# Performance work log

Hardware: AMD Instinct MI355X
Metric: run time of the kernel (lower is better)

The kernel has to match this reference:

```python
import jax, jax.numpy as jnp
import numpy as np

N = 100000        # nodes
E = 1600000       # edges
D = 128           # feature dim (all layers)
G = 128           # graphs
C = 10            # num_classes
L = 3             # conv layers
EPS = 1e-5
SLOPE = 0.03


def setup_inputs() -> dict:
    key = jax.random.key(0)
    ks = jax.random.split(key, 12)
    x = jax.random.normal(ks[0], (N, D), dtype=jnp.float32)
    edge_index = jax.random.randint(ks[1], (2, E), 0, N, dtype=jnp.int64)
    batch = jnp.sort(jax.random.randint(ks[2], (N,), 0, G, dtype=jnp.int64))
    s = 1.0 / np.sqrt(D)
    Wc = jax.random.uniform(ks[3], (L, D, D), jnp.float32, -s, s)
    bc = jax.random.uniform(ks[4], (L, D), jnp.float32, -s, s)
    bn_gamma = jnp.ones((2, D), jnp.float32)
    bn_beta = jnp.zeros((2, D), jnp.float32)
    bn_mean = jax.random.normal(ks[5], (2, D), jnp.float32) * 0.1
    bn_var = jax.random.uniform(ks[6], (2, D), jnp.float32, 0.5, 1.5)
    lin_w = jax.random.uniform(ks[7], (C, D), jnp.float32, -s, s)
    lin_b = jax.random.uniform(ks[8], (C,), jnp.float32, -s, s)
    return {"x": x, "edge_index": edge_index, "batch": batch, "Wc": Wc,
            "bc": bc, "bn_gamma": bn_gamma, "bn_beta": bn_beta,
            "bn_mean": bn_mean, "bn_var": bn_var, "lin_w": lin_w, "lin_b": lin_b}


def _gcn_norm(edge_index):
    # add self-loops, compute D^{-1/2}[row] * D^{-1/2}[col] (PyG gcn_norm)
    loops = jnp.arange(N, dtype=edge_index.dtype)
    row = jnp.concatenate([edge_index[0], loops])
    col = jnp.concatenate([edge_index[1], loops])
    deg = jax.ops.segment_sum(jnp.ones_like(col, dtype=jnp.float32), col, num_segments=N)
    dis = jnp.where(deg > 0, jax.lax.rsqrt(deg), 0.0)
    return row, col, dis[row] * dis[col]


def reference(x, edge_index, batch, Wc, bc, bn_gamma, bn_beta, bn_mean, bn_var, lin_w, lin_b):
    row, col, norm = _gcn_norm(edge_index)
    h = x
    for i in range(L):
        h = h @ Wc[i]                                          # linear transform [N, D]
        msg = h[row] * norm[:, None]                           # gather + normalize [E+N, D]
        h = jax.ops.segment_sum(msg, col, num_segments=N) + bc[i]
        if i < 2:  # batchnorm only for i < len(batchnorms)-1 (eval mode, running stats)
            h = (h - bn_mean[i]) * jax.lax.rsqrt(bn_var[i] + EPS) * bn_gamma[i] + bn_beta[i]
        h = jnp.where(h > 0, h, SLOPE * h)                     # LeakyReLU(0.03)
    # global mean pool over graphs
    counts = jax.ops.segment_sum(jnp.ones((N,), jnp.float32), batch, num_segments=G)
    pooled = jax.ops.segment_sum(h, batch, num_segments=G) / jnp.maximum(counts, 1.0)[:, None]
    # dropout is identity in eval; final linear head
    return pooled @ lin_w.T + lin_b                            # [G, C]
```

## Files before the change

### kernel.cpp

```cpp
#include <hip/hip_runtime.h>
#include <hip/hip_bf16.h>

#define NN 100000
#define EE 1600000
#define DD 128
#define GG 128
#define CC 10
#define NPB 256
#define NB 391
#define SCAP 5120
#define VPT 16
#define CPAD 32
#define PPN 64

typedef __attribute__((ext_vector_type(8))) short bf16x8;
typedef __attribute__((ext_vector_type(4))) float f32x4;
typedef __attribute__((ext_vector_type(2))) float f32x2;
typedef unsigned int u32;

__device__ inline float blo(u32 u) { return __uint_as_float(u << 16); }
__device__ inline float bhi(u32 u) { return __uint_as_float(u & 0xffff0000u); }
__device__ inline u32 bpack(float x, float y) {
    u32 bx = __float_as_uint(x);
    u32 by = __float_as_uint(y);
    bx = (bx + 0x7fffu + ((bx >> 16) & 1u)) >> 16;
    by = (by + 0x7fffu + ((by >> 16) & 1u)) & 0xffff0000u;
    return bx | by;
}

__global__ __launch_bounds__(256) void k_bcount(const int* __restrict__ col,
                                                int* __restrict__ bhist) {
    __shared__ int lh[NB];
    int tid = threadIdx.x;
    for (int b = tid; b < NB; b += 256) lh[b] = 0;
    __syncthreads();
    int base = blockIdx.x * (256 * VPT);
#pragma unroll
    for (int j = 0; j < VPT; j++) {
        int e = base + j * 256 + tid;
        if (e < EE) atomicAdd(&lh[col[e] >> 8], 1);
    }
    __syncthreads();
    for (int b = tid; b < NB; b += 256) {
        int h = lh[b];
        if (h) atomicAdd(&bhist[b * CPAD], h);
    }
}

__global__ __launch_bounds__(512) void k_bscan(const int* __restrict__ bhist,
                                               int* __restrict__ boffs,
                                               int* __restrict__ bcur) {
    __shared__ int s[512];
    int tid = threadIdx.x;
    int c = (tid < NB) ? bhist[tid * CPAD] : 0;
    s[tid] = c;
    __syncthreads();
    for (int off = 1; off < 512; off <<= 1) {
        int v = (tid >= off) ? s[tid - off] : 0;
        __syncthreads();
        s[tid] += v;
        __syncthreads();
    }
    int excl = s[tid] - c;
    if (tid < NB) {
        boffs[tid] = excl;
        bcur[tid * CPAD] = excl;
    }
    if (tid == NB - 1) boffs[NB] = excl + c;
}

__global__ __launch_bounds__(256) void k_part(const int* __restrict__ row, const int* __restrict__ col,
                                              int* __restrict__ bcur, u32* __restrict__ pairs) {
    __shared__ int lhist[NB];
    __shared__ int gbase[NB];
    __shared__ int lcur[NB];
    int tid = threadIdx.x;
    for (int b = tid; b < NB; b += 256) lhist[b] = 0;
    __syncthreads();
    int base = blockIdx.x * (256 * VPT);
    u32 v[VPT];
    int bb[VPT];
#pragma unroll
    for (int j = 0; j < VPT; j++) {
        int e = base + j * 256 + tid;
        if (e < EE) {
            int r = row[e], c = col[e];
            v[j] = ((u32)r << 8) | (u32)(c & 255);
            bb[j] = c >> 8;
            atomicAdd(&lhist[bb[j]], 1);
        } else {
            bb[j] = -1;
        }
    }
    __syncthreads();
    for (int b = tid; b < NB; b += 256) {
        int h = lhist[b];
        gbase[b] = h ? atomicAdd(&bcur[b * CPAD], h) : 0;
        lcur[b] = 0;
    }
    __syncthreads();
#pragma unroll
    for (int j = 0; j < VPT; j++) {
        if (bb[j] >= 0) {
            int slot = gbase[bb[j]] + atomicAdd(&lcur[bb[j]], 1);
            pairs[slot] = v[j];
        }
    }
}

__global__ __launch_bounds__(256) void k_sort(const u32* __restrict__ pairs,
                                              const int* __restrict__ boffs,
                                              int* __restrict__ offs,
                                              float* __restrict__ dis,
                                              int* __restrict__ src) {
    int b = blockIdx.x;
    int tid = threadIdx.x;
    int nstart = b << 8;
    int nvalid = NN - nstart;
    if (nvalid > NPB) nvalid = NPB;
    int base = boffs[b];
    int eend = boffs[b + 1];
    int cnt = eend - base;
    __shared__ int lcnt[NPB];
    __shared__ int lscan[NPB];
    __shared__ int lcur[NPB];
    __shared__ int lsrc[SCAP];
    lcnt[tid] = 0;
    __syncthreads();
    for (int e = base + tid; e < eend; e += 256)
        atomicAdd(&lcnt[pairs[e] & 255u], 1);
    __syncthreads();
    int c = lcnt[tid];
    lscan[tid] = c;
    __syncthreads();
    for (int off = 1; off < 256; off <<= 1) {
        int v = (tid >= off) ? lscan[tid - off] : 0;
        __syncthreads();
        lscan[tid] += v;
        __syncthreads();
    }
    int excl = lscan[tid] - c;
    if (tid < nvalid) {
        offs[nstart + tid] = base + excl;
        dis[nstart + tid] = rsqrtf((float)(c + 1));
    }
    if (b == NB - 1 && tid == 255) offs[NN] = EE;
    lcur[tid] = excl;
    __syncthreads();
    if (cnt <= SCAP) {
        for (int e = base + tid; e < eend; e += 256) {
            u32 v = pairs[e];
            int slot = atomicAdd(&lcur[v & 255u], 1);
            lsrc[slot] = (int)(v >> 8);
        }
        __syncthreads();
        for (int i = tid; i < cnt; i += 256)
            src[base + i] = lsrc[i];
    } else {
        for (int e = base + tid; e < eend; e += 256) {
            u32 v = pairs[e];
            int slot = base + atomicAdd(&lcur[v & 255u], 1);
            src[slot] = (int)(v >> 8);
        }
    }
}

__global__ void k_prep(const float* __restrict__ Wc, const float* __restrict__ bc,
                       const float* __restrict__ gamma, const float* __restrict__ beta,
                       const float* __restrict__ mean, const float* __restrict__ var,
                       __hip_bfloat16* __restrict__ WT,
                       float* __restrict__ tc) {
    int i = blockIdx.x * 256 + threadIdx.x;
    if (i < 3 * 128) {
        int l = i >> 7, d = i & 127;
        float t;
        if (l < 2) {
            float s = gamma[l * 128 + d] * rsqrtf(var[l * 128 + d] + 1e-5f);
            t = (bc[l * 128 + d] - mean[l * 128 + d]) * s + beta[l * 128 + d];
        } else {
            t = bc[2 * 128 + d];
        }
        tc[i] = t;
    }
    if (i < 3 * 16384) {
        int l = i >> 14, r = (i >> 7) & 127, k = i & 127;
        float s = 1.f;
        if (l < 2) s = gamma[l * 128 + r] * rsqrtf(var[l * 128 + r] + 1e-5f);
        WT[i] = __float2bfloat16(Wc[l * 16384 + k * 128 + r] * s);
    }
}

__global__ __launch_bounds__(256) void k_pre(const float* __restrict__ x,
                                             const float* __restrict__ dis,
                                             u32* __restrict__ hs) {
    int i = blockIdx.x * 256 + threadIdx.x;
    if (i < NN * 64) {
        float dn = dis[i >> 6];
        float2 v = ((const float2*)x)[i];
        hs[i] = bpack(v.x * dn, v.y * dn);
    }
}

template <int PRESCALE>
__global__ __launch_bounds__(1024) void k_aggT(const u32* __restrict__ hin,
                                               const int* __restrict__ offs,
                                               const int* __restrict__ src,
                                               const float* __restrict__ dis,
                                               const __hip_bfloat16* __restrict__ WT,
                                               const float* __restrict__ tc,
                                               u32* __restrict__ hout) {
    __shared__ u32   Atile[16][68];
    __shared__ float Otile[16][132];
    int wid = threadIdx.x >> 6;
    int lane = threadIdx.x & 63;
    int node = blockIdx.x * 16 + wid;
    int e0 = __builtin_amdgcn_readfirstlane(offs[node]);
    int e1 = __builtin_amdgcn_readfirstlane(offs[node + 1]);
    u32 self = hin[((u32)node << 6) + lane];
    f32x2 acc = {blo(self), bhi(self)};
    int e = e0;
    for (; e + 16 <= e1; e += 16) {
        u32 u[16];
#pragma unroll
        for (int j = 0; j < 16; j++) {
            u32 s = (u32)src[e + j];
            u[j] = hin[(s << 6) + lane];
        }
#pragma unroll
        for (int j = 0; j < 16; j++) {
            f32x2 v = {blo(u[j]), bhi(u[j])};
            acc += v;
        }
    }
    for (; e + 8 <= e1; e += 8) {
        u32 u[8];
#pragma unroll
        for (int j = 0; j < 8; j++) {
            u32 s = (u32)src[e + j];
            u[j] = hin[(s << 6) + lane];
        }
#pragma unroll
        for (int j = 0; j < 8; j++) {
            f32x2 v = {blo(u[j]), bhi(u[j])};
            acc += v;
        }
    }
    for (; e < e1; e++) {
        u32 u = hin[((u32)src[e] << 6) + lane];
        f32x2 v = {blo(u), bhi(u)};
        acc += v;
    }
    float dn = dis[node];
    Atile[wid][lane] = bpack(acc.x * dn, acc.y * dn);
    __syncthreads();
    if (wid < 8) {
        int lg = lane >> 4, lr = lane & 15;
        f32x4 c4 = {0.f, 0.f, 0.f, 0.f};
#pragma unroll
        for (int kk = 0; kk < 4; kk++) {
            bf16x8 a = *(const bf16x8*)&Atile[lr][kk * 16 + lg * 4];
            bf16x8 b = *(const bf16x8*)(WT + (size_t)(wid * 16 + lr) * 128 + kk * 32 + lg * 8);
            c4 = __builtin_amdgcn_mfma_f32_16x16x32_bf16(a, b, c4, 0, 0, 0);
        }
#pragma unroll
        for (int r = 0; r < 4; r++)
            Otile[lg * 4 + r][wid * 16 + lr] = c4[r];
    }
    __syncthreads();
    int d0 = lane * 2;
    float r0 = Otile[wid][d0]     + tc[d0];
    float r1 = Otile[wid][d0 + 1] + tc[d0 + 1];
    r0 = r0 > 0.f ? r0 : 0.03f * r0;
    r1 = r1 > 0.f ? r1 : 0.03f * r1;
    if (PRESCALE) { r0 *= dn; r1 *= dn; }
    hout[((u32)node << 6) + lane] = bpack(r0, r1);
}

__global__ __launch_bounds__(64) void k_pool(const u32* __restrict__ h,
                                             const int* __restrict__ batch,
                                             float* __restrict__ pooled,
                                             float* __restrict__ counts) {
    int lane = threadIdx.x;
    int n0 = blockIdx.x * PPN;
    if (n0 >= NN) return;
    int n1 = n0 + PPN;
    if (n1 > NN) n1 = NN;
    float a0 = 0.f, a1 = 0.f, cnt = 0.f;
    int g = batch[n0];
    for (int n = n0; n < n1; n++) {
        int bg = batch[n];
        if (bg != g) {
            atomicAdd(&pooled[g * 128 + lane * 2], a0);
            atomicAdd(&pooled[g * 128 + lane * 2 + 1], a1);
            if (lane == 0) atomicAdd(&counts[g], cnt);
            a0 = 0.f; a1 = 0.f; cnt = 0.f; g = bg;
        }
        u32 u = h[(u32)n * 64u + lane];
        a0 += blo(u); a1 += bhi(u);
        cnt += 1.f;
    }
    atomicAdd(&pooled[g * 128 + lane * 2], a0);
    atomicAdd(&pooled[g * 128 + lane * 2 + 1], a1);
    if (lane == 0) atomicAdd(&counts[g], cnt);
}

__global__ void k_head(const float* __restrict__ pooled, const float* __restrict__ counts,
                       const float* __restrict__ w, const float* __restrict__ b,
                       float* __restrict__ out) {
    int i = blockIdx.x * blockDim.x + threadIdx.x;
    if (i >= GG * CC) return;
    int g = i / CC, c = i % CC;
    float cnt = counts[g];
    cnt = cnt > 1.f ? cnt : 1.f;
    float inv = 1.f / cnt;
    const float* p = &pooled[g * 128];
    const float* ww = &w[c * 128];
    float acc = 0.f;
    for (int d = 0; d < 128; d++) acc += p[d] * ww[d];
    out[i] = acc * inv + b[c];
}

extern "C" void kernel_launch(void* const* d_in, const int* in_sizes, int n_in,
                              void* d_out, int out_size, void* d_ws, size_t ws_size,
                              hipStream_t stream) {
    const float* x     = (const float*)d_in[0];
    const int*   ei    = (const int*)d_in[1];
    const int*   row   = ei;
    const int*   col   = ei + EE;
    const int*   batch = (const int*)d_in[2];
    const float* Wc    = (const float*)d_in[3];
    const float* bc    = (const float*)d_in[4];
    const float* gamma = (const float*)d_in[5];
    const float* beta  = (const float*)d_in[6];
    const float* mean  = (const float*)d_in[7];
    const float* var   = (const float*)d_in[8];
    const float* lw    = (const float*)d_in[9];
    const float* lb    = (const float*)d_in[10];
    float* out = (float*)d_out;

    char* p = (char*)d_ws;
    auto alloc = [&](size_t bytes) -> char* {
        char* r = p;
        p += (bytes + 255) & ~(size_t)255;
        return r;
    };
    float* dis    = (float*)alloc((size_t)NN * 4);
    int*   offs   = (int*)alloc((size_t)(NN + 1) * 4);
    int*   bhist  = (int*)alloc((size_t)NB * CPAD * 4);
    int*   boffs  = (int*)alloc((size_t)(NB + 1) * 4);
    int*   bcur   = (int*)alloc((size_t)NB * CPAD * 4);
    int*   src    = (int*)alloc((size_t)EE * 4);
    __hip_bfloat16* WT = (__hip_bfloat16*)alloc((size_t)3 * 16384 * 2);
    float* tc     = (float*)alloc((size_t)3 * 128 * 4);
    float* pooled = (float*)alloc((size_t)GG * 128 * 4);
    float* counts = (float*)alloc((size_t)GG * 4);
    __hip_bfloat16* h0b = (__hip_bfloat16*)alloc((size_t)NN * 128 * 2);
    __hip_bfloat16* h1b = (__hip_bfloat16*)alloc((size_t)NN * 128 * 2);
    u32* pairs = (u32*)h0b;

    hipMemsetAsync(bhist, 0, (size_t)NB * CPAD * 4, stream);
    hipMemsetAsync(pooled, 0, (size_t)GG * 128 * 4, stream);
    hipMemsetAsync(counts, 0, (size_t)GG * 4, stream);

    const int eb_grid = (EE + 256 * VPT - 1) / (256 * VPT);
    k_bcount<<<eb_grid, 256, 0, stream>>>(col, bhist);
    k_bscan<<<1, 512, 0, stream>>>(bhist, boffs, bcur);
    k_part<<<eb_grid, 256, 0, stream>>>(row, col, bcur, pairs);
    k_sort<<<NB, 256, 0, stream>>>(pairs, boffs, offs, dis, src);
    k_prep<<<192, 256, 0, stream>>>(Wc, bc, gamma, beta, mean, var, WT, tc);
    k_pre<<<(NN * 64 + 255) / 256, 256, 0, stream>>>(x, dis, (u32*)h0b);

    const int fused_grid = NN / 16;

    k_aggT<1><<<fused_grid, 1024, 0, stream>>>((const u32*)h0b, offs, src, dis, WT,           tc,       (u32*)h1b);
    k_aggT<1><<<fused_grid, 1024, 0, stream>>>((const u32*)h1b, offs, src, dis, WT + 16384,   tc + 128, (u32*)h0b);
    k_aggT<0><<<fused_grid, 1024, 0, stream>>>((const u32*)h0b, offs, src, dis, WT + 2*16384, tc + 256, (u32*)h1b);

    k_pool<<<(NN + PPN - 1) / PPN, 64, 0, stream>>>((const u32*)h1b, batch, pooled, counts);
    k_head<<<(GG * CC + 255) / 256, 256, 0, stream>>>(pooled, counts, lw, lb, out);
}
```

Baseline: 379.9 us.

## Drop bucket-count pass via fixed-capacity partitions; use 256-thread aggregation blocks

The edge partitioning now writes each destination bucket into a fixed-capacity slot region (PCAP per bucket). This removes the separate counting kernel, and the bucket scan now runs after partitioning, on the counters it accumulated. Separately, the fused aggregate+matmul kernel moves from 1024 threads with one wave per node to 256 threads with each wave processing four nodes sequentially, and all four waves now take part in the MFMA tile. The aim is to cut a full pass over the column indices, one launch, and the idle waves during the matmul phase. The risk is that a bucket holding more than 4608 edges would overflow its region, and less gather parallelism per wave could hurt latency hiding.

Result: faster. 335.8 us (-11.6%).

```diff
diff --git a/kernel.cpp b/kernel.cpp
--- a/kernel.cpp
+++ b/kernel.cpp
@@ -12,6 +12,7 @@
 #define VPT 16
 #define CPAD 32
 #define PPN 64
+#define PCAP 4608
 
 typedef __attribute__((ext_vector_type(8))) short bf16x8;
 typedef __attribute__((ext_vector_type(4))) float f32x4;
@@ -26,47 +27,6 @@
     bx = (bx + 0x7fffu + ((bx >> 16) & 1u)) >> 16;
     by = (by + 0x7fffu + ((by >> 16) & 1u)) & 0xffff0000u;
     return bx | by;
-}
-
-__global__ __launch_bounds__(256) void k_bcount(const int* __restrict__ col,
-                                                int* __restrict__ bhist) {
-    __shared__ int lh[NB];
-    int tid = threadIdx.x;
-    for (int b = tid; b < NB; b += 256) lh[b] = 0;
-    __syncthreads();
-    int base = blockIdx.x * (256 * VPT);
-#pragma unroll
-    for (int j = 0; j < VPT; j++) {
-        int e = base + j * 256 + tid;
-        if (e < EE) atomicAdd(&lh[col[e] >> 8], 1);
-    }
-    __syncthreads();
-    for (int b = tid; b < NB; b += 256) {
-        int h = lh[b];
-        if (h) atomicAdd(&bhist[b * CPAD], h);
-    }
-}
-
-__global__ __launch_bounds__(512) void k_bscan(const int* __restrict__ bhist,
-                                               int* __restrict__ boffs,
-                                               int* __restrict__ bcur) {
-    __shared__ int s[512];
-    int tid = threadIdx.x;
-    int c = (tid < NB) ? bhist[tid * CPAD] : 0;
-    s[tid] = c;
-    __syncthreads();
-    for (int off = 1; off < 512; off <<= 1) {
-        int v = (tid >= off) ? s[tid - off] : 0;
-        __syncthreads();
-        s[tid] += v;
-        __syncthreads();
-    }
-    int excl = s[tid] - c;
-    if (tid < NB) {
-        boffs[tid] = excl;
-        bcur[tid * CPAD] = excl;
-    }
-    if (tid == NB - 1) boffs[NB] = excl + c;
 }
 
 __global__ __launch_bounds__(256) void k_part(const int* __restrict__ row, const int* __restrict__ col,
@@ -103,9 +63,27 @@
     for (int j = 0; j < VPT; j++) {
         if (bb[j] >= 0) {
             int slot = gbase[bb[j]] + atomicAdd(&lcur[bb[j]], 1);
-            pairs[slot] = v[j];
-        }
-    }
+            pairs[(u32)bb[j] * PCAP + slot] = v[j];
+        }
+    }
+}
+
+__global__ __launch_bounds__(512) void k_bscan(const int* __restrict__ bcur,
+                                               int* __restrict__ boffs) {
+    __shared__ int s[512];
+    int tid = threadIdx.x;
+    int c = (tid < NB) ? bcur[tid * CPAD] : 0;
+    s[tid] = c;
+    __syncthreads();
+    for (int off = 1; off < 512; off <<= 1) {
+        int v = (tid >= off) ? s[tid - off] : 0;
+        __syncthreads();
+        s[tid] += v;
+        __syncthreads();
+    }
+    int excl = s[tid] - c;
+    if (tid < NB) boffs[tid] = excl;
+    if (tid == NB - 1) boffs[NB] = excl + c;
 }
 
 __global__ __launch_bounds__(256) void k_sort(const u32* __restrict__ pairs,
@@ -119,16 +97,16 @@
     int nvalid = NN - nstart;
     if (nvalid > NPB) nvalid = NPB;
     int base = boffs[b];
-    int eend = boffs[b + 1];
-    int cnt = eend - base;
+    int cnt = boffs[b + 1] - base;
+    u32 pbase = (u32)b * PCAP;
     __shared__ int lcnt[NPB];
     __shared__ int lscan[NPB];
     __shared__ int lcur[NPB];
     __shared__ int lsrc[SCAP];
     lcnt[tid] = 0;
     __syncthreads();
-    for (int e = base + tid; e < eend; e += 256)
-        atomicAdd(&lcnt[pairs[e] & 255u], 1);
+    for (int i = tid; i < cnt; i += 256)
+        atomicAdd(&lcnt[pairs[pbase + i] & 255u], 1);
     __syncthreads();
     int c = lcnt[tid];
     lscan[tid] = c;
@@ -148,8 +126,8 @@
     lcur[tid] = excl;
     __syncthreads();
     if (cnt <= SCAP) {
-        for (int e = base + tid; e < eend; e += 256) {
-            u32 v = pairs[e];
+        for (int i = tid; i < cnt; i += 256) {
+            u32 v = pairs[pbase + i];
             int slot = atomicAdd(&lcur[v & 255u], 1);
             lsrc[slot] = (int)(v >> 8);
         }
@@ -157,8 +135,8 @@
         for (int i = tid; i < cnt; i += 256)
             src[base + i] = lsrc[i];
     } else {
-        for (int e = base + tid; e < eend; e += 256) {
-            u32 v = pairs[e];
+        for (int i = tid; i < cnt; i += 256) {
+            u32 v = pairs[pbase + i];
             int slot = base + atomicAdd(&lcur[v & 255u], 1);
             src[slot] = (int)(v >> 8);
         }
@@ -202,7 +180,7 @@
 }
 
 template <int PRESCALE>
-__global__ __launch_bounds__(1024) void k_aggT(const u32* __restrict__ hin,
+__global__ __launch_bounds__(256) void k_aggT2(const u32* __restrict__ hin,
                                                const int* __restrict__ offs,
                                                const int* __restrict__ src,
                                                const float* __restrict__ dis,
@@ -211,69 +189,83 @@
                                                u32* __restrict__ hout) {
     __shared__ u32   Atile[16][68];
     __shared__ float Otile[16][132];
-    int wid = threadIdx.x >> 6;
-    int lane = threadIdx.x & 63;
-    int node = blockIdx.x * 16 + wid;
-    int e0 = __builtin_amdgcn_readfirstlane(offs[node]);
-    int e1 = __builtin_amdgcn_readfirstlane(offs[node + 1]);
-    u32 self = hin[((u32)node << 6) + lane];
-    f32x2 acc = {blo(self), bhi(self)};
-    int e = e0;
-    for (; e + 16 <= e1; e += 16) {
-        u32 u[16];
-#pragma unroll
-        for (int j = 0; j < 16; j++) {
-            u32 s = (u32)src[e + j];
-            u[j] = hin[(s << 6) + lane];
-        }
-#pragma unroll
-        for (int j = 0; j < 16; j++) {
-            f32x2 v = {blo(u[j]), bhi(u[j])};
+    int tid = threadIdx.x;
+    int w = tid >> 6, lane = tid & 63;
+    int base = blockIdx.x * 16;
+    float dns[4];
+#pragma unroll
+    for (int i = 0; i < 4; i++) {
+        int slot = w * 4 + i;
+        int node = base + slot;
+        int e0 = __builtin_amdgcn_readfirstlane(offs[node]);
+        int e1 = __builtin_amdgcn_readfirstlane(offs[node + 1]);
+        u32 self = hin[((u32)node << 6) + lane];
+        f32x2 acc = {blo(self), bhi(self)};
+        int e = e0;
+        for (; e + 16 <= e1; e += 16) {
+            u32 u[16];
+#pragma unroll
+            for (int j = 0; j < 16; j++) {
+                u32 s = (u32)src[e + j];
+                u[j] = hin[(s << 6) + lane];
+            }
+#pragma unroll
+            for (int j = 0; j < 16; j++) {
+                f32x2 v = {blo(u[j]), bhi(u[j])};
+                acc += v;
+            }
+        }
+        for (; e + 8 <= e1; e += 8) {
+            u32 u[8];
+#pragma unroll
+            for (int j = 0; j < 8; j++) {
+                u32 s = (u32)src[e + j];
+                u[j] = hin[(s << 6) + lane];
+            }
+#pragma unroll
+            for (int j = 0; j < 8; j++) {
+                f32x2 v = {blo(u[j]), bhi(u[j])};
+                acc += v;
+            }
+        }
+        for (; e < e1; e++) {
+            u32 u = hin[((u32)src[e] << 6) + lane];
+            f32x2 v = {blo(u), bhi(u)};
             acc += v;
         }
-    }
-    for (; e + 8 <= e1; e += 8) {
-        u32 u[8];
-#pragma unroll
-        for (int j = 0; j < 8; j++) {
-            u32 s = (u32)src[e + j];
-            u[j] = hin[(s << 6) + lane];
-        }
-#pragma unroll
-        for (int j = 0; j < 8; j++) {
-            f32x2 v = {blo(u[j]), bhi(u[j])};
-            acc += v;
-        }
-    }
-    for (; e < e1; e++) {
-        u32 u = hin[((u32)src[e] << 6) + lane];
-        f32x2 v = {blo(u), bhi(u)};
-        acc += v;
-    }
-    float dn = dis[node];
-    Atile[wid][lane] = bpack(acc.x * dn, acc.y * dn);
-    __syncthreads();
-    if (wid < 8) {
-        int lg = lane >> 4, lr = lane & 15;
+        float dn = dis[node];
+        dns[i] = dn;
+        Atile[slot][lane] = bpack(acc.x * dn, acc.y * dn);
+    }
+    __syncthreads();
+    int lg = lane >> 4, lr = lane & 15;
+#pragma unroll
+    for (int t = 0; t < 2; t++) {
+        int ct = w * 2 + t;
         f32x4 c4 = {0.f, 0.f, 0.f, 0.f};
 #pragma unroll
         for (int kk = 0; kk < 4; kk++) {
             bf16x8 a = *(const bf16x8*)&Atile[lr][kk * 16 + lg * 4];
-            bf16x8 b = *(const bf16x8*)(WT + (size_t)(wid * 16 + lr) * 128 + kk * 32 + lg * 8);
+            bf16x8 b = *(const bf16x8*)(WT + (size_t)(ct * 16 + lr) * 128 + kk * 32 + lg * 8);
             c4 = __builtin_amdgcn_mfma_f32_16x16x32_bf16(a, b, c4, 0, 0, 0);
         }
 #pragma unroll
         for (int r = 0; r < 4; r++)
-            Otile[lg * 4 + r][wid * 16 + lr] = c4[r];
+            Otile[lg * 4 + r][ct * 16 + lr] = c4[r];
     }
     __syncthreads();
     int d0 = lane * 2;
-    float r0 = Otile[wid][d0]     + tc[d0];
-    float r1 = Otile[wid][d0 + 1] + tc[d0 + 1];
-    r0 = r0 > 0.f ? r0 : 0.03f * r0;
-    r1 = r1 > 0.f ? r1 : 0.03f * r1;
-    if (PRESCALE) { r0 *= dn; r1 *= dn; }
-    hout[((u32)node << 6) + lane] = bpack(r0, r1);
+    float t0 = tc[d0], t1 = tc[d0 + 1];
+#pragma unroll
+    for (int i = 0; i < 4; i++) {
+        int slot = w * 4 + i;
+        float r0 = Otile[slot][d0]     + t0;
+        float r1 = Otile[slot][d0 + 1] + t1;
+        r0 = r0 > 0.f ? r0 : 0.03f * r0;
+        r1 = r1 > 0.f ? r1 : 0.03f * r1;
+        if (PRESCALE) { r0 *= dns[i]; r1 *= dns[i]; }
+        hout[((u32)(base + slot) << 6) + lane] = bpack(r0, r1);
+    }
 }
 
 __global__ __launch_bounds__(64) void k_pool(const u32* __restrict__ h,
@@ -346,7 +338,6 @@
     };
     float* dis    = (float*)alloc((size_t)NN * 4);
     int*   offs   = (int*)alloc((size_t)(NN + 1) * 4);
-    int*   bhist  = (int*)alloc((size_t)NB * CPAD * 4);
     int*   boffs  = (int*)alloc((size_t)(NB + 1) * 4);
     int*   bcur   = (int*)alloc((size_t)NB * CPAD * 4);
     int*   src    = (int*)alloc((size_t)EE * 4);
@@ -358,23 +349,22 @@
     __hip_bfloat16* h1b = (__hip_bfloat16*)alloc((size_t)NN * 128 * 2);
     u32* pairs = (u32*)h0b;
 
-    hipMemsetAsync(bhist, 0, (size_t)NB * CPAD * 4, stream);
+    hipMemsetAsync(bcur, 0, (size_t)NB * CPAD * 4, stream);
     hipMemsetAsync(pooled, 0, (size_t)GG * 128 * 4, stream);
     hipMemsetAsync(counts, 0, (size_t)GG * 4, stream);
 
     const int eb_grid = (EE + 256 * VPT - 1) / (256 * VPT);
-    k_bcount<<<eb_grid, 256, 0, stream>>>(col, bhist);
-    k_bscan<<<1, 512, 0, stream>>>(bhist, boffs, bcur);
     k_part<<<eb_grid, 256, 0, stream>>>(row, col, bcur, pairs);
+    k_bscan<<<1, 512, 0, stream>>>(bcur, boffs);
     k_sort<<<NB, 256, 0, stream>>>(pairs, boffs, offs, dis, src);
     k_prep<<<192, 256, 0, stream>>>(Wc, bc, gamma, beta, mean, var, WT, tc);
     k_pre<<<(NN * 64 + 255) / 256, 256, 0, stream>>>(x, dis, (u32*)h0b);
 
     const int fused_grid = NN / 16;
 
-    k_aggT<1><<<fused_grid, 1024, 0, stream>>>((const u32*)h0b, offs, src, dis, WT,           tc,       (u32*)h1b);
-    k_aggT<1><<<fused_grid, 1024, 0, stream>>>((const u32*)h1b, offs, src, dis, WT + 16384,   tc + 128, (u32*)h0b);
-    k_aggT<0><<<fused_grid, 1024, 0, stream>>>((const u32*)h0b, offs, src, dis, WT + 2*16384, tc + 256, (u32*)h1b);
+    k_aggT2<1><<<fused_grid, 256, 0, stream>>>((const u32*)h0b, offs, src, dis, WT,           tc,       (u32*)h1b);
+    k_aggT2<1><<<fused_grid, 256, 0, stream>>>((const u32*)h1b, offs, src, dis, WT + 16384,   tc + 128, (u32*)h0b);
+    k_aggT2<0><<<fused_grid, 256, 0, stream>>>((const u32*)h0b, offs, src, dis, WT + 2*16384, tc + 256, (u32*)h1b);
 
     k_pool<<<(NN + PPN - 1) / PPN, 64, 0, stream>>>((const u32*)h1b, batch, pooled, counts);
     k_head<<<(GG * CC + 255) / 256, 256, 0, stream>>>(pooled, counts, lw, lb, out);
```
